# Optimization experiments

Hardware: AMD Instinct MI355X
Metric: run time of the kernel (lower is better)

The kernel has to match this reference:

```python
import jax, jax.numpy as jnp
import numpy as np

B, N, F_IN, F_OUT, E = 2, 8192, 64, 64, 262144
ALPHA = 0.2  # LeakyReLU negative slope


def setup_inputs() -> dict:
    key = jax.random.key(0)
    k1, k2, k3, k4, k5 = jax.random.split(key, 5)
    h = jax.random.normal(k1, (B, N, F_IN), dtype=jnp.float32)
    edge_index = jax.random.randint(k2, (2, E), 0, N, dtype=jnp.int64)
    edge_weight = jax.random.uniform(k3, (E,), dtype=jnp.float32)
    # torch Linear(in,out,bias=False): weight shape (out, in)
    lim_w = float(np.sqrt(1.0 / F_IN))
    W = jax.random.uniform(k4, (F_OUT, F_IN), minval=-lim_w, maxval=lim_w, dtype=jnp.float32)
    # xavier_uniform on (2*out, 1)
    lim_a = float(np.sqrt(6.0 / (2 * F_OUT + 1)))
    a = jax.random.uniform(k5, (2 * F_OUT, 1), minval=-lim_a, maxval=lim_a, dtype=jnp.float32)
    return {"h": h, "W": W, "a": a, "edge_index": edge_index, "edge_weight": edge_weight}


def reference(h, W, a, edge_index, edge_weight):
    src, dst = edge_index[0], edge_index[1]

    def single(hb):  # hb: (N, F_IN)
        Wh = hb @ W.T  # (N, F_OUT)
        edge_h = jnp.concatenate([Wh[src], Wh[dst]], axis=1)  # (E, 2*F_OUT)
        e = jax.nn.leaky_relu((edge_h @ a)[:, 0], negative_slope=ALPHA)  # (E,)
        e = e * edge_weight
        # dense N x N attention, zeros treated as masked (faithful to source)
        attn = jnp.zeros((N, N), dtype=Wh.dtype).at[src, dst].set(e)
        mask = attn == 0
        attn = jnp.where(mask, -jnp.inf, attn)
        attn = jax.nn.softmax(attn, axis=1)
        attn = jnp.where(mask, 0.0, attn)
        h_prime = attn @ Wh  # (N, F_OUT)
        return jax.nn.elu(h_prime)  # concat=True path

    return jax.vmap(single)(h)
```

## Files before the change

### kernel.cpp

```cpp
#include <hip/hip_runtime.h>
#include <hip/hip_bf16.h>
#include <math.h>

#define NN     8192
#define FDIM   64
#define EDGES  262144
#define BATCH  2
#define ALPHA  0.2f

#define NB     256
#define SRCB   32
#define BCAP   1280
#define ROWCAP 128

#define OFF_WH    0u
#define OFF_S1    4194304u
#define OFF_S2    4259840u
#define OFF_OFFS  4325376u
#define OFF_CRS   4456448u

__global__ __launch_bounds__(1024) void stage1_kernel(
    const float* __restrict__ h, const float* __restrict__ W,
    const float* __restrict__ a, const int* __restrict__ ei,
    float* __restrict__ Wh, float* __restrict__ s1, float* __restrict__ s2,
    unsigned short* __restrict__ offsT, uint2* __restrict__ coarse) {
  __shared__ float sW[64 * 65];
  __shared__ float sH[64 * 64];
  __shared__ int hist[NB];
  __shared__ int offs[NB];
  int tid = threadIdx.x, lane = tid & 63, w = tid >> 6;
  int blk = blockIdx.x;

  int e = blk * 1024 + tid;
  int s = ei[e], d = ei[EDGES + e];
  int g = s >> 5;
  if (tid < NB) hist[tid] = 0;
  __syncthreads();
  int rank = atomicAdd(&hist[g], 1);
  __syncthreads();
  if (tid < 64) {
    int i0 = tid * 4;
    int c0 = hist[i0], c1 = hist[i0 + 1], c2 = hist[i0 + 2], c3 = hist[i0 + 3];
    int sum = c0 + c1 + c2 + c3;
    int x = sum;
#pragma unroll
    for (int off = 1; off < 64; off <<= 1) {
      int y = __shfl_up(x, off, 64);
      if (tid >= off) x += y;
    }
    int ex = x - sum;
    offs[i0] = ex; offs[i0 + 1] = ex + c0;
    offs[i0 + 2] = ex + c0 + c1; offs[i0 + 3] = ex + c0 + c1 + c2;
  }
  __syncthreads();
  coarse[blk * 1024 + offs[g] + rank] =
      make_uint2(((unsigned)e << 13) | (unsigned)d, (unsigned)s);
  if (tid < NB) offsT[tid * 256 + blk] = (unsigned short)offs[tid];

  for (int i = tid; i < 4096; i += 1024) sW[(i >> 6) * 65 + (i & 63)] = W[i];
  int rr = lane >> 4, c4 = lane & 15;
  int nn0 = blk * 64 + w * 4;
  *(float4*)(sH + (w * 4 + rr) * 64 + c4 * 4) =
      *(const float4*)(h + (size_t)(nn0 + rr) * 64 + c4 * 4);
  __syncthreads();

  const float* wp = sW + lane * 65;
  const float* hp = sH + (w * 4) * 64;
  float acc[4] = {0.f, 0.f, 0.f, 0.f};
#pragma unroll 8
  for (int k = 0; k < 64; ++k) {
    float wv = wp[k];
    acc[0] += hp[k] * wv;
    acc[1] += hp[64 + k] * wv;
    acc[2] += hp[128 + k] * wv;
    acc[3] += hp[192 + k] * wv;
  }
  float a1 = a[lane], a2 = a[64 + lane];
#pragma unroll
  for (int r = 0; r < 4; ++r) {
    int nn = nn0 + r;
    Wh[(size_t)nn * 64 + lane] = acc[r];
    float p1 = acc[r] * a1, p2 = acc[r] * a2;
#pragma unroll
    for (int off = 32; off; off >>= 1) {
      p1 += __shfl_xor(p1, off, 64);
      p2 += __shfl_xor(p2, off, 64);
    }
    if (lane == 0) { s1[nn] = p1; s2[nn] = p2; }
  }
}

__global__ __launch_bounds__(1024) void stage2_kernel(
    const float* __restrict__ ew, const float* __restrict__ s1,
    const float* __restrict__ s2, const unsigned short* __restrict__ offsT,
    const uint2* __restrict__ coarse, const float* __restrict__ Wh,
    float* __restrict__ out) {
  __shared__ uint2 grp[BCAP];
  __shared__ int dstBase[257];
  __shared__ int srcPos[256];
  __shared__ int rhist[SRCB];
  __shared__ int roffs[SRCB];
  int tid = threadIdx.x, lane = tid & 63, w = tid >> 6;
  int blk = blockIdx.x;
  int xcd = blk & 7;
  int b = xcd >> 2;
  int g = (blk >> 3) * 4 + (xcd & 3);
  const float* s1b = s1 + b * NN;
  const float* s2b = s2 + b * NN;
  if (tid < SRCB) rhist[tid] = 0;

  if (tid < 256) {
    int lo = offsT[g * 256 + tid];
    int hi = (g == 255) ? 1024 : offsT[(g + 1) * 256 + tid];
    srcPos[tid] = tid * 1024 + lo;
    dstBase[tid] = hi - lo;
  }
  __syncthreads();
  if (tid < 64) {
    int i0 = tid * 4;
    int c0 = dstBase[i0], c1 = dstBase[i0 + 1], c2 = dstBase[i0 + 2], c3 = dstBase[i0 + 3];
    int sum = c0 + c1 + c2 + c3;
    int x = sum;
#pragma unroll
    for (int off = 1; off < 64; off <<= 1) {
      int y = __shfl_up(x, off, 64);
      if (tid >= off) x += y;
    }
    int ex = x - sum;
    dstBase[i0] = ex; dstBase[i0 + 1] = ex + c0;
    dstBase[i0 + 2] = ex + c0 + c1; dstBase[i0 + 3] = ex + c0 + c1 + c2;
    if (tid == 63) dstBase[256] = x;
  }
  __syncthreads();
  int T = dstBase[256]; if (T > BCAP) T = BCAP;

  unsigned mpk[2]; float mv[2]; int msl[2], mrk[2]; bool mok[2];
#pragma unroll
  for (int j = 0; j < 2; ++j) {
    int i = tid + j * 1024;
    mok[j] = (i < T);
    mpk[j] = 0; mv[j] = 0.f; msl[j] = 0; mrk[j] = 0;
    if (mok[j]) {
      int lo = 0, hi = 255;
#pragma unroll
      for (int st = 0; st < 8; ++st) {
        int mid = (lo + hi + 1) >> 1;
        if (dstBase[mid] <= i) lo = mid; else hi = mid - 1;
      }
      int c = lo, jj = i - dstBase[c];
      uint2 E = coarse[srcPos[c] + jj];
      int dst = (int)(E.x & 0x1FFFu);
      int eid = (int)(E.x >> 13);
      int src = (int)E.y;
      float x = s1b[src] + s2b[dst];
      float val = (x > 0.f ? x : ALPHA * x) * ew[eid];
      mpk[j] = E.x; mv[j] = val; msl[j] = src & (SRCB - 1);
      mrk[j] = atomicAdd(&rhist[msl[j]], 1);
    }
  }
  __syncthreads();
  if (tid < SRCB) {
    int c = rhist[tid];
    int x = c;
#pragma unroll
    for (int off = 1; off < SRCB; off <<= 1) {
      int y = __shfl_up(x, off, 64);
      if (tid >= off) x += y;
    }
    roffs[tid] = x - c;
  }
  __syncthreads();
#pragma unroll
  for (int j = 0; j < 2; ++j)
    if (mok[j]) grp[roffs[msl[j]] + mrk[j]] = make_uint2(mpk[j], __float_as_uint(mv[j]));
  __syncthreads();

  const float* Whb = Wh + (size_t)b * NN * FDIM;
  int fg = lane & 15, es = lane >> 4;
  for (int q = 0; q < 2; ++q) {
    int slo = w * 2 + q;
    int beg = roffs[slo];
    int deg = rhist[slo];
    int n = g * SRCB + slo;
    float4 r4 = make_float4(0.f, 0.f, 0.f, 0.f);
    if (deg > 0) {
      float inv;
      if (deg <= 64) {
        unsigned k0 = 0; float v0 = 0.f;
        if (lane < deg) { uint2 E = grp[beg + lane]; k0 = E.x; v0 = __uint_as_float(E.y); }
        for (int j = 0; j < deg; ++j) {
          unsigned q2 = __shfl(k0, j, 64);
          if ((((q2 ^ k0) & 0x1FFFu) == 0u) & (q2 > k0)) v0 = 0.f;
        }
        float m = (v0 != 0.f) ? v0 : -INFINITY;
#pragma unroll
        for (int off = 32; off; off >>= 1) m = fmaxf(m, __shfl_xor(m, off, 64));
        float p = (v0 != 0.f) ? expf(v0 - m) : 0.f;
        float sum = p;
#pragma unroll
        for (int off = 32; off; off >>= 1) sum += __shfl_xor(sum, off, 64);
        inv = (sum > 0.f) ? 1.f / sum : 0.f;
        if (lane < deg) grp[beg + lane].y = __float_as_uint(p);
      } else {
        int dg = deg > ROWCAP ? ROWCAP : deg;
        deg = dg;
        unsigned k0 = 0, k1 = 0; float v0 = 0.f, v1 = 0.f;
        { uint2 E = grp[beg + lane]; k0 = E.x; v0 = __uint_as_float(E.y); }
        if (lane + 64 < dg) { uint2 E = grp[beg + lane + 64]; k1 = E.x; v1 = __uint_as_float(E.y); }
        for (int j = 0; j < 64; ++j) {
          unsigned q2 = __shfl(k0, j, 64);
          if ((((q2 ^ k0) & 0x1FFFu) == 0u) & (q2 > k0)) v0 = 0.f;
          if ((((q2 ^ k1) & 0x1FFFu) == 0u) & (q2 > k1)) v1 = 0.f;
        }
        for (int j = 0; j < dg - 64; ++j) {
          unsigned q2 = __shfl(k1, j, 64);
          if ((((q2 ^ k0) & 0x1FFFu) == 0u) & (q2 > k0)) v0 = 0.f;
          if ((((q2 ^ k1) & 0x1FFFu) == 0u) & (q2 > k1)) v1 = 0.f;
        }
        float m = fmaxf((v0 != 0.f) ? v0 : -INFINITY, (v1 != 0.f) ? v1 : -INFINITY);
#pragma unroll
        for (int off = 32; off; off >>= 1) m = fmaxf(m, __shfl_xor(m, off, 64));
        float p0 = (v0 != 0.f) ? expf(v0 - m) : 0.f;
        float p1 = (v1 != 0.f) ? expf(v1 - m) : 0.f;
        float sum = p0 + p1;
#pragma unroll
        for (int off = 32; off; off >>= 1) sum += __shfl_xor(sum, off, 64);
        inv = (sum > 0.f) ? 1.f / sum : 0.f;
        grp[beg + lane].y = __float_as_uint(p0);
        if (lane + 64 < dg) grp[beg + lane + 64].y = __float_as_uint(p1);
      }
      float4 acc = make_float4(0.f, 0.f, 0.f, 0.f);
      for (int kk = 0; kk < deg; kk += 32) {
        float4 vv[8]; float pp[8];
#pragma unroll
        for (int u = 0; u < 8; ++u) {
          int k = kk + u * 4 + es;
          int kc = k < deg ? k : deg - 1;
          uint2 E = grp[beg + kc];
          pp[u] = (k < deg) ? __uint_as_float(E.y) : 0.f;
          vv[u] = *((const float4*)(Whb + (E.x & 0x1FFFu) * 64) + fg);
        }
#pragma unroll
        for (int u = 0; u < 8; ++u) {
          acc.x += pp[u] * vv[u].x; acc.y += pp[u] * vv[u].y;
          acc.z += pp[u] * vv[u].z; acc.w += pp[u] * vv[u].w;
        }
      }
#pragma unroll
      for (int off = 16; off <= 32; off <<= 1) {
        acc.x += __shfl_xor(acc.x, off, 64);
        acc.y += __shfl_xor(acc.y, off, 64);
        acc.z += __shfl_xor(acc.z, off, 64);
        acc.w += __shfl_xor(acc.w, off, 64);
      }
      r4.x = acc.x * inv; r4.y = acc.y * inv; r4.z = acc.z * inv; r4.w = acc.w * inv;
    }
    if (es == 0) {
      r4.x = r4.x > 0.f ? r4.x : expm1f(r4.x);
      r4.y = r4.y > 0.f ? r4.y : expm1f(r4.y);
      r4.z = r4.z > 0.f ? r4.z : expm1f(r4.z);
      r4.w = r4.w > 0.f ? r4.w : expm1f(r4.w);
      *((float4*)(out + ((size_t)b * NN + n) * 64) + fg) = r4;
    }
  }
}

extern "C" void kernel_launch(void* const* d_in, const int* in_sizes, int n_in,
                              void* d_out, int out_size, void* d_ws, size_t ws_size,
                              hipStream_t stream) {
  const float* h  = (const float*)d_in[0];
  const float* W  = (const float*)d_in[1];
  const float* a  = (const float*)d_in[2];
  const int*   ei = (const int*)d_in[3];
  const float* ew = (const float*)d_in[4];
  float* out = (float*)d_out;

  char* ws = (char*)d_ws;
  float*          Wh    = (float*)(ws + OFF_WH);
  float*          s1    = (float*)(ws + OFF_S1);
  float*          s2    = (float*)(ws + OFF_S2);
  unsigned short* offsT = (unsigned short*)(ws + OFF_OFFS);
  uint2*          coarse = (uint2*)(ws + OFF_CRS);

  stage1_kernel<<<256, 1024, 0, stream>>>(h, W, a, ei, Wh, s1, s2, offsT, coarse);
  stage2_kernel<<<BATCH * NB, 1024, 0, stream>>>(ew, s1, s2, offsT, coarse, Wh, out);
}
```

Baseline: 107.3 us.

## Pre-sort edge weights in stage1, use LDS bitmap dedup, widen stage1 per-thread work

```diff
diff --git a/kernel.cpp b/kernel.cpp
--- a/kernel.cpp
+++ b/kernel.cpp
@@ -18,12 +18,15 @@
 #define OFF_S2    4259840u
 #define OFF_OFFS  4325376u
 #define OFF_CRS   4456448u
-
-__global__ __launch_bounds__(1024) void stage1_kernel(
+#define OFF_CEW   6553600u
+
+__global__ __launch_bounds__(512) void stage1_kernel(
     const float* __restrict__ h, const float* __restrict__ W,
     const float* __restrict__ a, const int* __restrict__ ei,
-    float* __restrict__ Wh, float* __restrict__ s1, float* __restrict__ s2,
-    unsigned short* __restrict__ offsT, uint2* __restrict__ coarse) {
+    const float* __restrict__ ew,
+    float* __restrict__ Wh, float* __restrict__ s1g, float* __restrict__ s2g,
+    unsigned short* __restrict__ offsT, uint2* __restrict__ coarse,
+    float* __restrict__ cew) {
   __shared__ float sW[64 * 65];
   __shared__ float sH[64 * 64];
   __shared__ int hist[NB];
@@ -31,12 +34,14 @@
   int tid = threadIdx.x, lane = tid & 63, w = tid >> 6;
   int blk = blockIdx.x;
 
-  int e = blk * 1024 + tid;
-  int s = ei[e], d = ei[EDGES + e];
-  int g = s >> 5;
+  int e0 = blk * 1024 + tid, e1 = e0 + 512;
+  int sa = ei[e0], da = ei[EDGES + e0];
+  int sb = ei[e1], db = ei[EDGES + e1];
+  int ga = sa >> 5, gb = sb >> 5;
   if (tid < NB) hist[tid] = 0;
   __syncthreads();
-  int rank = atomicAdd(&hist[g], 1);
+  int ra = atomicAdd(&hist[ga], 1);
+  int rb = atomicAdd(&hist[gb], 1);
   __syncthreads();
   if (tid < 64) {
     int i0 = tid * 4;
@@ -53,31 +58,41 @@
     offs[i0 + 2] = ex + c0 + c1; offs[i0 + 3] = ex + c0 + c1 + c2;
   }
   __syncthreads();
-  coarse[blk * 1024 + offs[g] + rank] =
-      make_uint2(((unsigned)e << 13) | (unsigned)d, (unsigned)s);
+  float wa = ew[e0], wb = ew[e1];
+  int pa = blk * 1024 + offs[ga] + ra;
+  int pb = blk * 1024 + offs[gb] + rb;
+  coarse[pa] = make_uint2(((unsigned)e0 << 13) | (unsigned)da, (unsigned)sa);
+  coarse[pb] = make_uint2(((unsigned)e1 << 13) | (unsigned)db, (unsigned)sb);
+  cew[pa] = wa;
+  cew[pb] = wb;
   if (tid < NB) offsT[tid * 256 + blk] = (unsigned short)offs[tid];
 
-  for (int i = tid; i < 4096; i += 1024) sW[(i >> 6) * 65 + (i & 63)] = W[i];
-  int rr = lane >> 4, c4 = lane & 15;
-  int nn0 = blk * 64 + w * 4;
-  *(float4*)(sH + (w * 4 + rr) * 64 + c4 * 4) =
-      *(const float4*)(h + (size_t)(nn0 + rr) * 64 + c4 * 4);
+  for (int i = tid; i < 4096; i += 512) sW[(i >> 6) * 65 + (i & 63)] = W[i];
+  int nn0 = blk * 64 + w * 8;
+#pragma unroll
+  for (int u = 0; u < 2; ++u) {
+    int idx = u * 64 + lane;
+    int r = idx >> 4, c = idx & 15;
+    *(float4*)(sH + (w * 8 + r) * 64 + c * 4) =
+        *(const float4*)(h + (size_t)(nn0 + r) * 64 + c * 4);
+  }
   __syncthreads();
 
   const float* wp = sW + lane * 65;
-  const float* hp = sH + (w * 4) * 64;
-  float acc[4] = {0.f, 0.f, 0.f, 0.f};
-#pragma unroll 8
-  for (int k = 0; k < 64; ++k) {
-    float wv = wp[k];
-    acc[0] += hp[k] * wv;
-    acc[1] += hp[64 + k] * wv;
-    acc[2] += hp[128 + k] * wv;
-    acc[3] += hp[192 + k] * wv;
+  const float* hp = sH + (w * 8) * 64;
+  float acc[8] = {0.f, 0.f, 0.f, 0.f, 0.f, 0.f, 0.f, 0.f};
+#pragma unroll
+  for (int k4 = 0; k4 < 16; ++k4) {
+    float w0 = wp[4 * k4], w1 = wp[4 * k4 + 1], w2 = wp[4 * k4 + 2], w3 = wp[4 * k4 + 3];
+#pragma unroll
+    for (int r = 0; r < 8; ++r) {
+      float4 hv = *(const float4*)(hp + r * 64 + k4 * 4);
+      acc[r] += hv.x * w0 + hv.y * w1 + hv.z * w2 + hv.w * w3;
+    }
   }
   float a1 = a[lane], a2 = a[64 + lane];
 #pragma unroll
-  for (int r = 0; r < 4; ++r) {
+  for (int r = 0; r < 8; ++r) {
     int nn = nn0 + r;
     Wh[(size_t)nn * 64 + lane] = acc[r];
     float p1 = acc[r] * a1, p2 = acc[r] * a2;
@@ -86,28 +101,32 @@
       p1 += __shfl_xor(p1, off, 64);
       p2 += __shfl_xor(p2, off, 64);
     }
-    if (lane == 0) { s1[nn] = p1; s2[nn] = p2; }
+    if (lane == 0) { s1g[nn] = p1; s2g[nn] = p2; }
   }
 }
 
 __global__ __launch_bounds__(1024) void stage2_kernel(
-    const float* __restrict__ ew, const float* __restrict__ s1,
-    const float* __restrict__ s2, const unsigned short* __restrict__ offsT,
-    const uint2* __restrict__ coarse, const float* __restrict__ Wh,
+    const float* __restrict__ s1g, const float* __restrict__ s2g,
+    const unsigned short* __restrict__ offsT, const uint2* __restrict__ coarse,
+    const float* __restrict__ cew, const float* __restrict__ Wh,
     float* __restrict__ out) {
   __shared__ uint2 grp[BCAP];
   __shared__ int dstBase[257];
   __shared__ int srcPos[256];
   __shared__ int rhist[SRCB];
   __shared__ int roffs[SRCB];
+  __shared__ unsigned bmap[16 * 256];
+  __shared__ float s1loc[SRCB];
   int tid = threadIdx.x, lane = tid & 63, w = tid >> 6;
   int blk = blockIdx.x;
   int xcd = blk & 7;
   int b = xcd >> 2;
   int g = (blk >> 3) * 4 + (xcd & 3);
-  const float* s1b = s1 + b * NN;
-  const float* s2b = s2 + b * NN;
-  if (tid < SRCB) rhist[tid] = 0;
+  const float* s2b = s2g + b * NN;
+  if (tid < SRCB) {
+    rhist[tid] = 0;
+    s1loc[tid] = s1g[b * NN + g * SRCB + tid];
+  }
 
   if (tid < 256) {
     int lo = offsT[g * 256 + tid];
@@ -149,11 +168,11 @@
       }
       int c = lo, jj = i - dstBase[c];
       uint2 E = coarse[srcPos[c] + jj];
+      float wgt = cew[srcPos[c] + jj];
       int dst = (int)(E.x & 0x1FFFu);
-      int eid = (int)(E.x >> 13);
       int src = (int)E.y;
-      float x = s1b[src] + s2b[dst];
-      float val = (x > 0.f ? x : ALPHA * x) * ew[eid];
+      float x = s1loc[src & (SRCB - 1)] + s2b[dst];
+      float val = (x > 0.f ? x : ALPHA * x) * wgt;
       mpk[j] = E.x; mv[j] = val; msl[j] = src & (SRCB - 1);
       mrk[j] = atomicAdd(&rhist[msl[j]], 1);
     }
@@ -176,6 +195,7 @@
   __syncthreads();
 
   const float* Whb = Wh + (size_t)b * NN * FDIM;
+  unsigned* mywords = bmap + w * 256;
   int fg = lane & 15, es = lane >> 4;
   for (int q = 0; q < 2; ++q) {
     int slo = w * 2 + q;
@@ -188,9 +208,19 @@
       if (deg <= 64) {
         unsigned k0 = 0; float v0 = 0.f;
         if (lane < deg) { uint2 E = grp[beg + lane]; k0 = E.x; v0 = __uint_as_float(E.y); }
-        for (int j = 0; j < deg; ++j) {
-          unsigned q2 = __shfl(k0, j, 64);
-          if ((((q2 ^ k0) & 0x1FFFu) == 0u) & (q2 > k0)) v0 = 0.f;
+#pragma unroll
+        for (int u = 0; u < 4; ++u) mywords[u * 64 + lane] = 0u;
+        bool dup = false;
+        if (lane < deg) {
+          int dst = (int)(k0 & 0x1FFFu);
+          unsigned old = atomicOr(&mywords[dst >> 5], 1u << (dst & 31));
+          dup = (old >> (dst & 31)) & 1u;
+        }
+        if (__ballot(dup) != 0ull) {
+          for (int j = 0; j < deg; ++j) {
+            unsigned q2 = __shfl(k0, j, 64);
+            if ((((q2 ^ k0) & 0x1FFFu) == 0u) & (q2 > k0)) v0 = 0.f;
+          }
         }
         float m = (v0 != 0.f) ? v0 : -INFINITY;
 #pragma unroll
@@ -276,12 +306,13 @@
   float* out = (float*)d_out;
 
   char* ws = (char*)d_ws;
-  float*          Wh    = (float*)(ws + OFF_WH);
-  float*          s1    = (float*)(ws + OFF_S1);
-  float*          s2    = (float*)(ws + OFF_S2);
-  unsigned short* offsT = (unsigned short*)(ws + OFF_OFFS);
+  float*          Wh     = (float*)(ws + OFF_WH);
+  float*          s1     = (float*)(ws + OFF_S1);
+  float*          s2     = (float*)(ws + OFF_S2);
+  unsigned short* offsT  = (unsigned short*)(ws + OFF_OFFS);
   uint2*          coarse = (uint2*)(ws + OFF_CRS);
-
-  stage1_kernel<<<256, 1024, 0, stream>>>(h, W, a, ei, Wh, s1, s2, offsT, coarse);
-  stage2_kernel<<<BATCH * NB, 1024, 0, stream>>>(ew, s1, s2, offsT, coarse, Wh, out);
+  float*          cew    = (float*)(ws + OFF_CEW);
+
+  stage1_kernel<<<256, 512, 0, stream>>>(h, W, a, ei, ew, Wh, s1, s2, offsT, coarse, cew);
+  stage2_kernel<<<BATCH * NB, 1024, 0, stream>>>(s1, s2, offsT, coarse, cew, Wh, out);
 }
```

Result: slower. 149.4 us (+39.2%).

## Pack edge weight into coarse records, drop LDS matmul, cache s1 per block

Applied to the files above, without the earlier changes.

```diff
diff --git a/kernel.cpp b/kernel.cpp
--- a/kernel.cpp
+++ b/kernel.cpp
@@ -22,10 +22,9 @@
 __global__ __launch_bounds__(1024) void stage1_kernel(
     const float* __restrict__ h, const float* __restrict__ W,
     const float* __restrict__ a, const int* __restrict__ ei,
-    float* __restrict__ Wh, float* __restrict__ s1, float* __restrict__ s2,
-    unsigned short* __restrict__ offsT, uint2* __restrict__ coarse) {
-  __shared__ float sW[64 * 65];
-  __shared__ float sH[64 * 64];
+    const float* __restrict__ ew,
+    float* __restrict__ Wh, float* __restrict__ s1g, float* __restrict__ s2g,
+    unsigned short* __restrict__ offsT, uint4* __restrict__ coarse) {
   __shared__ int hist[NB];
   __shared__ int offs[NB];
   int tid = threadIdx.x, lane = tid & 63, w = tid >> 6;
@@ -53,27 +52,28 @@
     offs[i0 + 2] = ex + c0 + c1; offs[i0 + 3] = ex + c0 + c1 + c2;
   }
   __syncthreads();
+  float wgt = ew[e];
   coarse[blk * 1024 + offs[g] + rank] =
-      make_uint2(((unsigned)e << 13) | (unsigned)d, (unsigned)s);
+      make_uint4(((unsigned)e << 13) | (unsigned)d, (unsigned)s,
+                 __float_as_uint(wgt), 0u);
   if (tid < NB) offsT[tid * 256 + blk] = (unsigned short)offs[tid];
 
-  for (int i = tid; i < 4096; i += 1024) sW[(i >> 6) * 65 + (i & 63)] = W[i];
-  int rr = lane >> 4, c4 = lane & 15;
+  float4 wreg[16];
+  {
+    const float4* W4 = (const float4*)(W + lane * 64);
+#pragma unroll
+    for (int i = 0; i < 16; ++i) wreg[i] = W4[i];
+  }
   int nn0 = blk * 64 + w * 4;
-  *(float4*)(sH + (w * 4 + rr) * 64 + c4 * 4) =
-      *(const float4*)(h + (size_t)(nn0 + rr) * 64 + c4 * 4);
-  __syncthreads();
-
-  const float* wp = sW + lane * 65;
-  const float* hp = sH + (w * 4) * 64;
   float acc[4] = {0.f, 0.f, 0.f, 0.f};
-#pragma unroll 8
-  for (int k = 0; k < 64; ++k) {
-    float wv = wp[k];
-    acc[0] += hp[k] * wv;
-    acc[1] += hp[64 + k] * wv;
-    acc[2] += hp[128 + k] * wv;
-    acc[3] += hp[192 + k] * wv;
+#pragma unroll
+  for (int k4 = 0; k4 < 16; ++k4) {
+#pragma unroll
+    for (int r = 0; r < 4; ++r) {
+      float4 hv = *((const float4*)(h + (size_t)(nn0 + r) * 64) + k4);
+      acc[r] += hv.x * wreg[k4].x + hv.y * wreg[k4].y +
+                hv.z * wreg[k4].z + hv.w * wreg[k4].w;
+    }
   }
   float a1 = a[lane], a2 = a[64 + lane];
 #pragma unroll
@@ -86,28 +86,30 @@
       p1 += __shfl_xor(p1, off, 64);
       p2 += __shfl_xor(p2, off, 64);
     }
-    if (lane == 0) { s1[nn] = p1; s2[nn] = p2; }
+    if (lane == 0) { s1g[nn] = p1; s2g[nn] = p2; }
   }
 }
 
 __global__ __launch_bounds__(1024) void stage2_kernel(
-    const float* __restrict__ ew, const float* __restrict__ s1,
-    const float* __restrict__ s2, const unsigned short* __restrict__ offsT,
-    const uint2* __restrict__ coarse, const float* __restrict__ Wh,
-    float* __restrict__ out) {
+    const float* __restrict__ s1g, const float* __restrict__ s2g,
+    const unsigned short* __restrict__ offsT, const uint4* __restrict__ coarse,
+    const float* __restrict__ Wh, float* __restrict__ out) {
   __shared__ uint2 grp[BCAP];
   __shared__ int dstBase[257];
   __shared__ int srcPos[256];
   __shared__ int rhist[SRCB];
   __shared__ int roffs[SRCB];
+  __shared__ float s1loc[SRCB];
   int tid = threadIdx.x, lane = tid & 63, w = tid >> 6;
   int blk = blockIdx.x;
   int xcd = blk & 7;
   int b = xcd >> 2;
   int g = (blk >> 3) * 4 + (xcd & 3);
-  const float* s1b = s1 + b * NN;
-  const float* s2b = s2 + b * NN;
-  if (tid < SRCB) rhist[tid] = 0;
+  const float* s2b = s2g + b * NN;
+  if (tid < SRCB) {
+    rhist[tid] = 0;
+    s1loc[tid] = s1g[b * NN + g * SRCB + tid];
+  }
 
   if (tid < 256) {
     int lo = offsT[g * 256 + tid];
@@ -148,12 +150,11 @@
         if (dstBase[mid] <= i) lo = mid; else hi = mid - 1;
       }
       int c = lo, jj = i - dstBase[c];
-      uint2 E = coarse[srcPos[c] + jj];
+      uint4 E = coarse[srcPos[c] + jj];
       int dst = (int)(E.x & 0x1FFFu);
-      int eid = (int)(E.x >> 13);
       int src = (int)E.y;
-      float x = s1b[src] + s2b[dst];
-      float val = (x > 0.f ? x : ALPHA * x) * ew[eid];
+      float x = s1loc[src & (SRCB - 1)] + s2b[dst];
+      float val = (x > 0.f ? x : ALPHA * x) * __uint_as_float(E.z);
       mpk[j] = E.x; mv[j] = val; msl[j] = src & (SRCB - 1);
       mrk[j] = atomicAdd(&rhist[msl[j]], 1);
     }
@@ -276,12 +277,12 @@
   float* out = (float*)d_out;
 
   char* ws = (char*)d_ws;
-  float*          Wh    = (float*)(ws + OFF_WH);
-  float*          s1    = (float*)(ws + OFF_S1);
-  float*          s2    = (float*)(ws + OFF_S2);
-  unsigned short* offsT = (unsigned short*)(ws + OFF_OFFS);
-  uint2*          coarse = (uint2*)(ws + OFF_CRS);
-
-  stage1_kernel<<<256, 1024, 0, stream>>>(h, W, a, ei, Wh, s1, s2, offsT, coarse);
-  stage2_kernel<<<BATCH * NB, 1024, 0, stream>>>(ew, s1, s2, offsT, coarse, Wh, out);
+  float*          Wh     = (float*)(ws + OFF_WH);
+  float*          s1     = (float*)(ws + OFF_S1);
+  float*          s2     = (float*)(ws + OFF_S2);
+  unsigned short* offsT  = (unsigned short*)(ws + OFF_OFFS);
+  uint4*          coarse = (uint4*)(ws + OFF_CRS);
+
+  stage1_kernel<<<256, 1024, 0, stream>>>(h, W, a, ei, ew, Wh, s1, s2, offsT, coarse);
+  stage2_kernel<<<BATCH * NB, 1024, 0, stream>>>(s1, s2, offsT, coarse, Wh, out);
 }
```

After: 191.6 us. 78.6% more time.
